# Kernel optimization log

Measured on AMD Instinct MI355X. Metric: run time of the kernel, lower is better.

Reference implementation:

```python
import jax, jax.numpy as jnp
import numpy as np

HUGE_INT = 1e31
EPSILON = float(np.finfo(np.float64).eps)

B, A, D = 256, 512, 200
AD = 3 * D  # action_dim
N_REL, N_ENT, N_TRIP = 500, 100000, 200000


def setup_inputs() -> dict:
    key = jax.random.key(0)
    ks = jax.random.split(key, 12)
    f32 = jnp.float32
    return {
        "obs": jax.random.normal(ks[0], (B, D), f32),
        "W1": jax.random.normal(ks[1], (D, AD), f32) / np.sqrt(D),
        "b1": jnp.zeros((AD,), f32),
        "W2": jax.random.normal(ks[2], (AD, AD), f32) / np.sqrt(AD),
        "b2": jnp.zeros((AD,), f32),
        "rel_emb": jax.random.normal(ks[3], (N_REL, D), f32),
        "ent_emb": jax.random.normal(ks[4], (N_ENT, D), f32),
        "trip_emb": jax.random.normal(ks[5], (N_TRIP, D), f32),
        "r_space": jax.random.randint(ks[6], (B, A), 0, N_REL, jnp.int32),
        "e_space": jax.random.randint(ks[7], (B, A), 0, N_ENT, jnp.int32),
        "triple_id": jax.random.randint(ks[8], (B, A), 0, N_TRIP, jnp.int32),
        "action_mask": jax.random.randint(ks[9], (B, A), 0, 2, jnp.int32),
    }


def reference(obs, W1, b1, W2, b2, rel_emb, ent_emb, trip_emb,
              r_space, e_space, triple_id, action_mask):
    # MLP on the question/state embedding (dropout = identity in eval mode)
    X2 = jnp.maximum(obs @ W1 + b1, 0.0) @ W2 + b2  # [B, 3D]
    # Gather action embeddings: concat(relation, entity, triple) -> [B, A, 3D]
    A_emb = jnp.concatenate(
        [rel_emb[r_space], ent_emb[e_space], trip_emb[triple_id]], axis=-1)
    mask = action_mask.astype(X2.dtype)
    # scores: squeeze(A @ X2[:, :, None]) - (1 - mask) * HUGE_INT
    logits = jnp.einsum("bad,bd->ba", A_emb, X2) - (1.0 - mask) * HUGE_INT
    action_dist = jax.nn.softmax(logits, axis=-1)  # [B, A]
    ent = jnp.sum(-action_dist * jnp.log(action_dist + EPSILON), axis=1)  # [B]
    return action_dist, ent
```

## Files before the change

kernel.cpp:

```cpp
#include <hip/hip_runtime.h>
#include <hip/hip_bf16.h>

#define BB 256
#define AA 512
#define DD 200
#define ADIM 600
#define NKC 4
#define KCH 150


__global__ __launch_bounds__(320) void k_x1(const float* __restrict__ obs,
                                            const float* __restrict__ W1,
                                            const float* __restrict__ b1,
                                            float* __restrict__ X1) {
  __shared__ __align__(16) float s_obs[2 * DD];
  const int rb = blockIdx.x * 2;
  const int tid = threadIdx.x;
  if (tid < 100) {
    reinterpret_cast<float4*>(s_obs)[tid] =
        reinterpret_cast<const float4*>(obs + rb * DD)[tid];
  }
  __syncthreads();

  const int jp = tid;
  if (jp < 300) {
    const int j0 = 2 * jp;
    float a00 = 0.f, a01 = 0.f, a10 = 0.f, a11 = 0.f;
#pragma unroll 5
    for (int kq = 0; kq < 50; ++kq) {
      const float4 x0 = *reinterpret_cast<const float4*>(&s_obs[kq * 4]);
      const float4 x1 = *reinterpret_cast<const float4*>(&s_obs[DD + kq * 4]);
      const float* wb = W1 + (kq * 4) * ADIM + j0;
      const float2 w0 = *reinterpret_cast<const float2*>(wb);
      const float2 w1 = *reinterpret_cast<const float2*>(wb + ADIM);
      const float2 w2 = *reinterpret_cast<const float2*>(wb + 2 * ADIM);
      const float2 w3 = *reinterpret_cast<const float2*>(wb + 3 * ADIM);
      a00 = fmaf(x0.x, w0.x, a00); a01 = fmaf(x0.x, w0.y, a01);
      a10 = fmaf(x1.x, w0.x, a10); a11 = fmaf(x1.x, w0.y, a11);
      a00 = fmaf(x0.y, w1.x, a00); a01 = fmaf(x0.y, w1.y, a01);
      a10 = fmaf(x1.y, w1.x, a10); a11 = fmaf(x1.y, w1.y, a11);
      a00 = fmaf(x0.z, w2.x, a00); a01 = fmaf(x0.z, w2.y, a01);
      a10 = fmaf(x1.z, w2.x, a10); a11 = fmaf(x1.z, w2.y, a11);
      a00 = fmaf(x0.w, w3.x, a00); a01 = fmaf(x0.w, w3.y, a01);
      a10 = fmaf(x1.w, w3.x, a10); a11 = fmaf(x1.w, w3.y, a11);
    }
    const float2 bv = *reinterpret_cast<const float2*>(b1 + j0);
    float2 o0, o1;
    o0.x = fmaxf(a00 + bv.x, 0.f); o0.y = fmaxf(a01 + bv.y, 0.f);
    o1.x = fmaxf(a10 + bv.x, 0.f); o1.y = fmaxf(a11 + bv.y, 0.f);
    *reinterpret_cast<float2*>(X1 + rb * ADIM + j0) = o0;
    *reinterpret_cast<float2*>(X1 + (rb + 1) * ADIM + j0) = o1;
  }
}

__global__ __launch_bounds__(640) void k_x2p(const float* __restrict__ X1,
                                             const float* __restrict__ W2,
                                             float* __restrict__ parts) {
  __shared__ __align__(16) float s_x1[4 * 152];
  const int rg = blockIdx.x >> 2;
  const int kc = blockIdx.x & 3;
  const int tid = threadIdx.x;
  const int kbase = kc * KCH;

  for (int idx = tid; idx < 4 * KCH; idx += 640) {
    const int r = idx / KCH, c = idx % KCH;
    s_x1[r * 152 + c] = X1[(rg * 4 + r) * ADIM + kbase + c];
  }
  __syncthreads();

  const int j = tid;
  if (j < ADIM) {
    float acc0 = 0.f, acc1 = 0.f, acc2 = 0.f, acc3 = 0.f;
#pragma unroll 4
    for (int kq = 0; kq < 37; ++kq) {
      const int k4 = kq * 4;
      const float4 x0 = *reinterpret_cast<const float4*>(&s_x1[0 * 152 + k4]);
      const float4 x1 = *reinterpret_cast<const float4*>(&s_x1[1 * 152 + k4]);
      const float4 x2 = *reinterpret_cast<const float4*>(&s_x1[2 * 152 + k4]);
      const float4 x3 = *reinterpret_cast<const float4*>(&s_x1[3 * 152 + k4]);
      const float* wb = W2 + (size_t)(kbase + k4) * ADIM + j;
      const float w0 = wb[0];
      const float w1 = wb[ADIM];
      const float w2 = wb[2 * ADIM];
      const float w3 = wb[3 * ADIM];
      acc0 = fmaf(x0.x, w0, fmaf(x0.y, w1, fmaf(x0.z, w2, fmaf(x0.w, w3, acc0))));
      acc1 = fmaf(x1.x, w0, fmaf(x1.y, w1, fmaf(x1.z, w2, fmaf(x1.w, w3, acc1))));
      acc2 = fmaf(x2.x, w0, fmaf(x2.y, w1, fmaf(x2.z, w2, fmaf(x2.w, w3, acc2))));
      acc3 = fmaf(x3.x, w0, fmaf(x3.y, w1, fmaf(x3.z, w2, fmaf(x3.w, w3, acc3))));
    }
#pragma unroll
    for (int kk = 148; kk < KCH; ++kk) {
      const float w = W2[(size_t)(kbase + kk) * ADIM + j];
      acc0 = fmaf(s_x1[0 * 152 + kk], w, acc0);
      acc1 = fmaf(s_x1[1 * 152 + kk], w, acc1);
      acc2 = fmaf(s_x1[2 * 152 + kk], w, acc2);
      acc3 = fmaf(s_x1[3 * 152 + kk], w, acc3);
    }
    float* pb = parts + (size_t)kc * (BB * ADIM) + (rg * 4) * ADIM + j;
    pb[0] = acc0;
    pb[ADIM] = acc1;
    pb[2 * ADIM] = acc2;
    pb[3 * ADIM] = acc3;
  }
}

__global__ __launch_bounds__(640) void k_x2(const float* __restrict__ parts,
                                            const float* __restrict__ b2,
                                            float* __restrict__ X2) {
  const int b = blockIdx.x;
  const int j = threadIdx.x;
  if (j < ADIM) {
    float v = b2[j];
#pragma unroll
    for (int kc = 0; kc < NKC; ++kc)
      v += parts[(size_t)kc * (BB * ADIM) + b * ADIM + j];
    X2[b * ADIM + j] = v;
  }
}

template <int CTRL>
__device__ inline float rot_add(float x) {
  const int xi = __float_as_int(x);
  const int r = __builtin_amdgcn_update_dpp(0, xi, CTRL, 0xF, 0xF, false);
  return x + __int_as_float(r);
}

__global__ __launch_bounds__(256, 6) void k_logits(
    const float* __restrict__ X2, const float* __restrict__ rel,
    const float* __restrict__ entt, const float* __restrict__ trip,
    const int* __restrict__ r_sp, const int* __restrict__ e_sp,
    const int* __restrict__ t_id, const int* __restrict__ amask,
    float* __restrict__ logits) {
  const int b = blockIdx.x >> 3;
  const int c = blockIdx.x & 7;
  const int w = threadIdx.x >> 6;
  const int lane = threadIdx.x & 63;
  const int base = b * AA + c * 64 + w * 16;

  float4 xr = {0.f, 0.f, 0.f, 0.f}, xe = xr, xt = xr;
  if (lane < 50) {
    const float* x2row = X2 + b * ADIM;
    xr = *reinterpret_cast<const float4*>(x2row + 4 * lane);
    xe = *reinterpret_cast<const float4*>(x2row + DD + 4 * lane);
    xt = *reinterpret_cast<const float4*>(x2row + 2 * DD + 4 * lane);
  }

  const int q = lane & 15;
  const int idxR = r_sp[base + q];
  const int idxE = e_sp[base + q];
  const int idxT = t_id[base + q];
  const int mk = amask[base + q];
  unsigned int mbits =
      (unsigned int)(__ballot(mk != 0) & 0xFFFFULL);

  const int lc = lane < 50 ? lane : 49;

  float pv = 0.0f;

  if (mbits) {
    int i0 = __builtin_ctz(mbits);
    mbits &= mbits - 1;
    float4 vr = *reinterpret_cast<const float4*>(
        rel + (size_t)__builtin_amdgcn_readlane(idxR, i0) * DD + 4 * lc);
    float4 ve = *reinterpret_cast<const float4*>(
        entt + (size_t)__builtin_amdgcn_readlane(idxE, i0) * DD + 4 * lc);
    float4 vt = *reinterpret_cast<const float4*>(
        trip + (size_t)__builtin_amdgcn_readlane(idxT, i0) * DD + 4 * lc);

    while (mbits) {
      const int i1 = __builtin_ctz(mbits);
      mbits &= mbits - 1;
      const float4 nr = *reinterpret_cast<const float4*>(
          rel + (size_t)__builtin_amdgcn_readlane(idxR, i1) * DD + 4 * lc);
      const float4 ne = *reinterpret_cast<const float4*>(
          entt + (size_t)__builtin_amdgcn_readlane(idxE, i1) * DD + 4 * lc);
      const float4 nt = *reinterpret_cast<const float4*>(
          trip + (size_t)__builtin_amdgcn_readlane(idxT, i1) * DD + 4 * lc);

      float p = fmaf(vr.x, xr.x, fmaf(vr.y, xr.y, fmaf(vr.z, xr.z, vr.w * xr.w)));
      p = fmaf(ve.x, xe.x, fmaf(ve.y, xe.y, fmaf(ve.z, xe.z, fmaf(ve.w, xe.w, p))));
      p = fmaf(vt.x, xt.x, fmaf(vt.y, xt.y, fmaf(vt.z, xt.z, fmaf(vt.w, xt.w, p))));
      p = rot_add<0x128>(p);
      p = rot_add<0x124>(p);
      p = rot_add<0x122>(p);
      p = rot_add<0x121>(p);
      pv = (q == i0) ? p + pv : pv;

      vr = nr; ve = ne; vt = nt;
      i0 = i1;
    }

    float p = fmaf(vr.x, xr.x, fmaf(vr.y, xr.y, fmaf(vr.z, xr.z, vr.w * xr.w)));
    p = fmaf(ve.x, xe.x, fmaf(ve.y, xe.y, fmaf(ve.z, xe.z, fmaf(ve.w, xe.w, p))));
    p = fmaf(vt.x, xt.x, fmaf(vt.y, xt.y, fmaf(vt.z, xt.z, fmaf(vt.w, xt.w, p))));
    p = rot_add<0x128>(p);
    p = rot_add<0x124>(p);
    p = rot_add<0x122>(p);
    p = rot_add<0x121>(p);
    pv = (q == i0) ? p + pv : pv;
  }

  const float u1 = pv + __shfl_xor(pv, 16);
  const float u2 = u1 + __shfl_xor(u1, 32);

  if (lane < 16) {
    logits[base + lane] = mk ? u2 : -1e31f;
  }
}

__device__ inline float waveMax(float v) {
#pragma unroll
  for (int o = 32; o > 0; o >>= 1) v = fmaxf(v, __shfl_xor(v, o));
  return v;
}
__device__ inline float waveSum(float v) {
#pragma unroll
  for (int o = 32; o > 0; o >>= 1) v += __shfl_xor(v, o);
  return v;
}

__global__ __launch_bounds__(512) void k_soft(const float* __restrict__ logits,
                                              float* __restrict__ out_dist,
                                              float* __restrict__ out_ent) {
  __shared__ float s_red[8];
  const int b = blockIdx.x;
  const int tid = threadIdx.x;
  const float logit = logits[b * AA + tid];

  float m = waveMax(logit);
  if ((tid & 63) == 0) s_red[tid >> 6] = m;
  __syncthreads();
  float bm = s_red[0];
#pragma unroll
  for (int w = 1; w < 8; ++w) bm = fmaxf(bm, s_red[w]);
  __syncthreads();

  const float ev = __expf(logit - bm);
  float s = waveSum(ev);
  if ((tid & 63) == 0) s_red[tid >> 6] = s;
  __syncthreads();
  float bs = 0.0f;
#pragma unroll
  for (int w = 0; w < 8; ++w) bs += s_red[w];

  const float p = ev / bs;
  out_dist[b * AA + tid] = p;

  const float term = -p * __logf(p + 2.220446049250313e-16f);
  __syncthreads();
  float es = waveSum(term);
  if ((tid & 63) == 0) s_red[tid >> 6] = es;
  __syncthreads();
  if (tid == 0) {
    float etot = 0.0f;
#pragma unroll
    for (int w = 0; w < 8; ++w) etot += s_red[w];
    out_ent[b] = etot;
  }
}

extern "C" void kernel_launch(void* const* d_in, const int* in_sizes, int n_in,
                              void* d_out, int out_size, void* d_ws, size_t ws_size,
                              hipStream_t stream) {
  const float* obs  = (const float*)d_in[0];
  const float* W1   = (const float*)d_in[1];
  const float* b1   = (const float*)d_in[2];
  const float* W2   = (const float*)d_in[3];
  const float* b2   = (const float*)d_in[4];
  const float* rel  = (const float*)d_in[5];
  const float* entt = (const float*)d_in[6];
  const float* trip = (const float*)d_in[7];
  const int* r_sp   = (const int*)d_in[8];
  const int* e_sp   = (const int*)d_in[9];
  const int* t_id   = (const int*)d_in[10];
  const int* amask  = (const int*)d_in[11];

  float* ws = (float*)d_ws;
  float* X1     = ws;
  float* parts  = ws + BB * ADIM;
  float* X2     = ws + BB * ADIM * (1 + NKC);
  float* logits = ws + BB * ADIM * (2 + NKC);

  float* out = (float*)d_out;

  k_x1<<<128, 320, 0, stream>>>(obs, W1, b1, X1);
  k_x2p<<<256, 640, 0, stream>>>(X1, W2, parts);
  k_x2<<<BB, 640, 0, stream>>>(parts, b2, X2);
  k_logits<<<BB * 8, 256, 0, stream>>>(X2, rel, entt, trip, r_sp, e_sp,
                                       t_id, amask, logits);
  k_soft<<<BB, 512, 0, stream>>>(logits, out, out + BB * AA);
}
```

Measured before the change: 51.72 us.

## Replace split-K partial buffer and reduce kernel with atomic accumulation into X2

```diff
diff --git a/kernel.cpp b/kernel.cpp
--- a/kernel.cpp
+++ b/kernel.cpp
@@ -12,50 +12,47 @@
 __global__ __launch_bounds__(320) void k_x1(const float* __restrict__ obs,
                                             const float* __restrict__ W1,
                                             const float* __restrict__ b1,
-                                            float* __restrict__ X1) {
-  __shared__ __align__(16) float s_obs[2 * DD];
-  const int rb = blockIdx.x * 2;
+                                            const float* __restrict__ b2,
+                                            float* __restrict__ X1,
+                                            float* __restrict__ X2) {
+  __shared__ __align__(16) float s_obs[DD];
+  const int b = blockIdx.x;
   const int tid = threadIdx.x;
-  if (tid < 100) {
+  for (int j = tid; j < ADIM; j += 320) X2[b * ADIM + j] = b2[j];
+  if (tid < 50) {
     reinterpret_cast<float4*>(s_obs)[tid] =
-        reinterpret_cast<const float4*>(obs + rb * DD)[tid];
+        reinterpret_cast<const float4*>(obs + b * DD)[tid];
   }
   __syncthreads();
 
   const int jp = tid;
   if (jp < 300) {
     const int j0 = 2 * jp;
-    float a00 = 0.f, a01 = 0.f, a10 = 0.f, a11 = 0.f;
+    float a0 = 0.f, a1 = 0.f;
 #pragma unroll 5
     for (int kq = 0; kq < 50; ++kq) {
-      const float4 x0 = *reinterpret_cast<const float4*>(&s_obs[kq * 4]);
-      const float4 x1 = *reinterpret_cast<const float4*>(&s_obs[DD + kq * 4]);
+      const float4 x = *reinterpret_cast<const float4*>(&s_obs[kq * 4]);
       const float* wb = W1 + (kq * 4) * ADIM + j0;
       const float2 w0 = *reinterpret_cast<const float2*>(wb);
       const float2 w1 = *reinterpret_cast<const float2*>(wb + ADIM);
       const float2 w2 = *reinterpret_cast<const float2*>(wb + 2 * ADIM);
       const float2 w3 = *reinterpret_cast<const float2*>(wb + 3 * ADIM);
-      a00 = fmaf(x0.x, w0.x, a00); a01 = fmaf(x0.x, w0.y, a01);
-      a10 = fmaf(x1.x, w0.x, a10); a11 = fmaf(x1.x, w0.y, a11);
-      a00 = fmaf(x0.y, w1.x, a00); a01 = fmaf(x0.y, w1.y, a01);
-      a10 = fmaf(x1.y, w1.x, a10); a11 = fmaf(x1.y, w1.y, a11);
-      a00 = fmaf(x0.z, w2.x, a00); a01 = fmaf(x0.z, w2.y, a01);
-      a10 = fmaf(x1.z, w2.x, a10); a11 = fmaf(x1.z, w2.y, a11);
-      a00 = fmaf(x0.w, w3.x, a00); a01 = fmaf(x0.w, w3.y, a01);
-      a10 = fmaf(x1.w, w3.x, a10); a11 = fmaf(x1.w, w3.y, a11);
+      a0 = fmaf(x.x, w0.x, a0); a1 = fmaf(x.x, w0.y, a1);
+      a0 = fmaf(x.y, w1.x, a0); a1 = fmaf(x.y, w1.y, a1);
+      a0 = fmaf(x.z, w2.x, a0); a1 = fmaf(x.z, w2.y, a1);
+      a0 = fmaf(x.w, w3.x, a0); a1 = fmaf(x.w, w3.y, a1);
     }
     const float2 bv = *reinterpret_cast<const float2*>(b1 + j0);
-    float2 o0, o1;
-    o0.x = fmaxf(a00 + bv.x, 0.f); o0.y = fmaxf(a01 + bv.y, 0.f);
-    o1.x = fmaxf(a10 + bv.x, 0.f); o1.y = fmaxf(a11 + bv.y, 0.f);
-    *reinterpret_cast<float2*>(X1 + rb * ADIM + j0) = o0;
-    *reinterpret_cast<float2*>(X1 + (rb + 1) * ADIM + j0) = o1;
+    float2 o;
+    o.x = fmaxf(a0 + bv.x, 0.f);
+    o.y = fmaxf(a1 + bv.y, 0.f);
+    *reinterpret_cast<float2*>(X1 + b * ADIM + j0) = o;
   }
 }
 
 __global__ __launch_bounds__(640) void k_x2p(const float* __restrict__ X1,
                                              const float* __restrict__ W2,
-                                             float* __restrict__ parts) {
+                                             float* __restrict__ X2) {
   __shared__ __align__(16) float s_x1[4 * 152];
   const int rg = blockIdx.x >> 2;
   const int kc = blockIdx.x & 3;
@@ -96,25 +93,11 @@
       acc2 = fmaf(s_x1[2 * 152 + kk], w, acc2);
       acc3 = fmaf(s_x1[3 * 152 + kk], w, acc3);
     }
-    float* pb = parts + (size_t)kc * (BB * ADIM) + (rg * 4) * ADIM + j;
-    pb[0] = acc0;
-    pb[ADIM] = acc1;
-    pb[2 * ADIM] = acc2;
-    pb[3 * ADIM] = acc3;
-  }
-}
-
-__global__ __launch_bounds__(640) void k_x2(const float* __restrict__ parts,
-                                            const float* __restrict__ b2,
-                                            float* __restrict__ X2) {
-  const int b = blockIdx.x;
-  const int j = threadIdx.x;
-  if (j < ADIM) {
-    float v = b2[j];
-#pragma unroll
-    for (int kc = 0; kc < NKC; ++kc)
-      v += parts[(size_t)kc * (BB * ADIM) + b * ADIM + j];
-    X2[b * ADIM + j] = v;
+    float* xb = X2 + (size_t)(rg * 4) * ADIM + j;
+    atomicAdd(&xb[0], acc0);
+    atomicAdd(&xb[ADIM], acc1);
+    atomicAdd(&xb[2 * ADIM], acc2);
+    atomicAdd(&xb[3 * ADIM], acc3);
   }
 }
 
@@ -277,15 +260,13 @@
 
   float* ws = (float*)d_ws;
   float* X1     = ws;
-  float* parts  = ws + BB * ADIM;
-  float* X2     = ws + BB * ADIM * (1 + NKC);
-  float* logits = ws + BB * ADIM * (2 + NKC);
+  float* X2     = ws + BB * ADIM;
+  float* logits = ws + 2 * BB * ADIM;
 
   float* out = (float*)d_out;
 
-  k_x1<<<128, 320, 0, stream>>>(obs, W1, b1, X1);
-  k_x2p<<<256, 640, 0, stream>>>(X1, W2, parts);
-  k_x2<<<BB, 640, 0, stream>>>(parts, b2, X2);
+  k_x1<<<BB, 320, 0, stream>>>(obs, W1, b1, b2, X1, X2);
+  k_x2p<<<256, 640, 0, stream>>>(X1, W2, X2);
   k_logits<<<BB * 8, 256, 0, stream>>>(X2, rel, entt, trip, r_sp, e_sp,
                                        t_id, amask, logits);
   k_soft<<<BB, 512, 0, stream>>>(logits, out, out + BB * AA);
```

Result: faster. 49.86 us (-3.6%).
